# Optimization experiments

Measured on AMD Instinct MI355X. Metric: run time of the kernel, lower is better.

Reference implementation:

```python
import jax, jax.numpy as jnp
import numpy as np

NQ = 100000  # Query nodes
NP = 100000  # Product nodes
E = 600000   # edges per relation
D_IN = 128
D_H = 128
# relation r: (src_type, dst_type); 0=Query, 1=Product
# 0: Click Q->P, 1: reverse_Click P->Q, 2: reverse_QueryResult P->Q, 3: QueryResult Q->P
REL = [(0, 1), (1, 0), (1, 0), (0, 1)]
N_NODES = [NQ, NP]


def setup_inputs() -> dict:
    key = jax.random.key(0)
    ks = jax.random.split(key, 12)
    s = 1.0 / np.sqrt(D_IN)  # keep activations well-scaled across 2 layers
    return {
        "x_query": jax.random.normal(ks[0], (NQ, D_IN), jnp.float32),
        "x_product": jax.random.normal(ks[1], (NP, D_IN), jnp.float32),
        "src_idx": jax.random.randint(ks[2], (4, E), 0, NQ, jnp.int32),
        "dst_idx": jax.random.randint(ks[3], (4, E), 0, NP, jnp.int32),
        "W_self1": jax.random.normal(ks[4], (4, D_IN, D_H), jnp.float32) * s,
        "W_neigh1": jax.random.normal(ks[5], (4, D_IN, D_H), jnp.float32) * s,
        "b1": jnp.zeros((4, D_H), jnp.float32),
        "W_self2": jax.random.normal(ks[6], (4, D_H, D_H), jnp.float32) * s,
        "W_neigh2": jax.random.normal(ks[7], (4, D_H, D_H), jnp.float32) * s,
        "b2": jnp.zeros((4, D_H), jnp.float32),
    }


def _hetero_sage_layer(h, W_self, W_neigh, b, src_idx, dst_idx):
    # h: [h_query, h_product]; per-relation SAGEConv(mean), cross-relation sum
    acc = [None, None]
    for r, (s, t) in enumerate(REL):
        nt = N_NODES[t]
        msg = h[s][src_idx[r]]                                   # [E, d] gather
        neigh_sum = jax.ops.segment_sum(msg, dst_idx[r], num_segments=nt)
        deg = jax.ops.segment_sum(jnp.ones((E,), h[s].dtype), dst_idx[r],
                                  num_segments=nt)
        neigh_mean = neigh_sum / jnp.maximum(deg, 1.0)[:, None]
        out = h[t] @ W_self[r] + neigh_mean @ W_neigh[r] + b[r]
        acc[t] = out if acc[t] is None else acc[t] + out
    return acc


def reference(x_query, x_product, src_idx, dst_idx,
              W_self1, W_neigh1, b1, W_self2, W_neigh2, b2):
    h = [x_query, x_product]
    h = _hetero_sage_layer(h, W_self1, W_neigh1, b1, src_idx, dst_idx)
    h = [jax.nn.relu(v) for v in h]  # ReLU only between layers
    h = _hetero_sage_layer(h, W_self2, W_neigh2, b2, src_idx, dst_idx)
    return (h[0], h[1])  # (H_query, H_product)
```

## Files before the change

kernel.cpp:

```cpp
#include <hip/hip_runtime.h>
#include <hip/hip_bf16.h>

#define N_NODES 100000
#define NEDGE   600000
#define BSHIFT  9
#define NBUCK   196
#define BCAP    3456
#define CGRID   6250
#define WGRID   96

typedef __attribute__((ext_vector_type(8))) short bf16x8;
typedef __attribute__((ext_vector_type(4))) short s16x4;
typedef __attribute__((ext_vector_type(4))) float f32x4;
typedef __attribute__((ext_vector_type(4))) unsigned u32x4;

__device__ __forceinline__ short f2bf(float f) {
  union { float f; unsigned u; } x; x.f = f;
  unsigned r = x.u + 0x7FFFu + ((x.u >> 16) & 1u);
  return (short)(r >> 16);
}

__device__ __forceinline__ unsigned cvtpk(float lo, float hi) {
  unsigned r;
  asm("v_cvt_pk_bf16_f32 %0, %1, %2" : "=v"(r) : "v"(lo), "v"(hi));
  return r;
}

__global__ __launch_bounds__(256) void bin_k(const int* __restrict__ sidx,
                                             const int* __restrict__ didx,
                                             int* __restrict__ bincnt,
                                             unsigned* __restrict__ stage) {
  __shared__ int hist[NBUCK];
  __shared__ int base[NBUCK];
  int r = blockIdx.y, t = threadIdx.x;
  int e0 = blockIdx.x * 2048 + t;
  const int* dd = didx + (size_t)r * NEDGE;
  const int* ss = sidx + (size_t)r * NEDGE;
  for (int i = t; i < NBUCK; i += 256) hist[i] = 0;
  __syncthreads();
  unsigned pv[8]; int bu[8], lr[8];
#pragma unroll
  for (int j = 0; j < 8; ++j) {
    int e = e0 + j * 256;
    if (e < NEDGE) {
      int dv = dd[e];
      bu[j] = dv >> BSHIFT;
      pv[j] = (unsigned)ss[e] | ((unsigned)(dv & 511) << 17);
      lr[j] = atomicAdd(&hist[bu[j]], 1);
    }
  }
  __syncthreads();
  for (int i = t; i < NBUCK; i += 256)
    base[i] = atomicAdd(&bincnt[r * NBUCK + i], hist[i]);
  __syncthreads();
#pragma unroll
  for (int j = 0; j < 8; ++j) {
    int e = e0 + j * 256;
    if (e < NEDGE)
      stage[(size_t)(r * NBUCK + bu[j]) * BCAP + base[bu[j]] + lr[j]] = pv[j];
  }
}

__global__ __launch_bounds__(256) void hist_k(const unsigned* __restrict__ stage,
                                              const int* __restrict__ bincnt,
                                              int* __restrict__ cnt,
                                              int* __restrict__ bucketsum) {
  __shared__ int h[512];
  __shared__ int red[256];
  int bu = blockIdx.x, r = blockIdx.y, t = threadIdx.x;
  int len = bincnt[r * NBUCK + bu];
  const unsigned* sg = stage + (size_t)(r * NBUCK + bu) * BCAP;
  h[t] = 0; h[t + 256] = 0;
  __syncthreads();
  for (int i = t; i < len; i += 256) atomicAdd(&h[sg[i] >> 17], 1);
  __syncthreads();
  int lo = bu << BSHIFT;
  int d0 = lo + t;
  if (d0 < N_NODES)       cnt[r * N_NODES + d0]       = h[t];
  if (d0 + 256 < N_NODES) cnt[r * N_NODES + d0 + 256] = h[t + 256];
  red[t] = h[t] + h[t + 256];
  __syncthreads();
  for (int st = 128; st > 0; st >>= 1) {
    if (t < st) red[t] += red[t + st];
    __syncthreads();
  }
  if (t == 0) bucketsum[r * NBUCK + bu] = red[0];
}

__global__ __launch_bounds__(256) void scan2_k(int* __restrict__ bucketsum) {
  __shared__ int buf[256];
  int t = threadIdx.x;
  for (int r = 0; r < 4; ++r) {
    int v = (t < NBUCK) ? bucketsum[r * NBUCK + t] : 0;
    buf[t] = v;
    __syncthreads();
    for (int st = 1; st < 256; st <<= 1) {
      int x = (t >= st) ? buf[t - st] : 0;
      __syncthreads();
      buf[t] += x;
      __syncthreads();
    }
    if (t < NBUCK) bucketsum[r * NBUCK + t] = buf[t] - v;
    __syncthreads();
  }
}

__global__ __launch_bounds__(256) void scan3_k(const int* __restrict__ cnt,
                                               const int* __restrict__ bucketsum,
                                               int* __restrict__ off) {
  __shared__ int ps[256];
  int bu = blockIdx.x, r = blockIdx.y, t = threadIdx.x;
  int lo = bu << BSHIFT;
  int i0 = lo + 2 * t;
  int c0 = (i0 < N_NODES) ? cnt[r * N_NODES + i0] : 0;
  int c1 = (i0 + 1 < N_NODES) ? cnt[r * N_NODES + i0 + 1] : 0;
  int pair = c0 + c1;
  ps[t] = pair;
  __syncthreads();
  for (int st = 1; st < 256; st <<= 1) {
    int x = (t >= st) ? ps[t - st] : 0;
    __syncthreads();
    ps[t] += x;
    __syncthreads();
  }
  int base = bucketsum[r * NBUCK + bu] + ps[t] - pair;
  int* o = off + r * (N_NODES + 1);
  if (i0 < N_NODES)     o[i0]     = base;
  if (i0 + 1 < N_NODES) o[i0 + 1] = base + c0;
  if (bu == 0 && t == 0) o[N_NODES] = NEDGE;
}

__global__ __launch_bounds__(256) void place_k(const unsigned* __restrict__ stage,
                                               const int* __restrict__ bincnt,
                                               const int* __restrict__ off,
                                               int* __restrict__ csr) {
  __shared__ int ofl[512];
  __shared__ int cur[512];
  int bu = blockIdx.x, r = blockIdx.y, t = threadIdx.x;
  int len = bincnt[r * NBUCK + bu];
  const unsigned* sg = stage + (size_t)(r * NBUCK + bu) * BCAP;
  const int* of = off + r * (N_NODES + 1);
  int* cs = csr + (size_t)r * NEDGE;
  int lo = bu << BSHIFT;
  int d0 = lo + t;
  ofl[t]       = (d0 < N_NODES) ? of[d0] : 0;
  ofl[t + 256] = (d0 + 256 < N_NODES) ? of[d0 + 256] : 0;
  cur[t] = 0; cur[t + 256] = 0;
  __syncthreads();
  for (int i = t; i < len; i += 256) {
    unsigned v = sg[i];
    int dl = v >> 17;
    int pos = ofl[dl] + atomicAdd(&cur[dl], 1);
    cs[pos] = (int)(v & 0x1FFFFu);
  }
}

__global__ __launch_bounds__(256) void fatprep_k(
    const float* __restrict__ xq, const float* __restrict__ xp,
    unsigned* __restrict__ xqb, unsigned* __restrict__ xpb,
    const float* __restrict__ Ws1, const float* __restrict__ Wn1,
    const float* __restrict__ Ws2, const float* __restrict__ Wn2,
    short* __restrict__ WTp,
    const float* __restrict__ b1, const float* __restrict__ b2,
    float* __restrict__ biasc) {
  int b = blockIdx.x, t = threadIdx.x;
  if (b < 2 * CGRID) {
    const float* x = (b < CGRID) ? xq : xp;
    unsigned* o = (b < CGRID) ? xqb : xpb;
    int i = (b < CGRID ? b : b - CGRID) * 256 + t;
    f32x4 v0 = ((const f32x4*)x)[i * 2];
    f32x4 v1 = ((const f32x4*)x)[i * 2 + 1];
    ((u32x4*)o)[i] = (u32x4){cvtpk(v0[0], v0[1]), cvtpk(v0[2], v0[3]),
                             cvtpk(v1[0], v1[1]), cvtpk(v1[2], v1[3])};
  } else if (b < 2 * CGRID + WGRID) {
    int tid = (b - 2 * CGRID) * 256 + t;
    int lane = tid & 63;
    int n0 = (tid >> 6) & 7;
    int idx3 = tid >> 9;
    int k0 = idx3 % 12;
    int lt = idx3 / 12;
    int l = lt >> 1, ty = lt & 1;
    const float* Wself  = l ? Ws2 : Ws1;
    const float* Wneigh = l ? Wn2 : Wn1;
    int rA = ty ? 0 : 1, rB = ty ? 3 : 2;
    int n = n0 * 16 + (lane & 15);
    int kbase = k0 * 32 + (lane >> 4) * 8;
    short out[8];
#pragma unroll
    for (int j = 0; j < 8; ++j) {
      int k = kbase + j;
      int kk = k & 127, blk = k >> 7;
      float v;
      if (blk == 0)      v = Wself[rA * 16384 + kk * 128 + n] + Wself[rB * 16384 + kk * 128 + n];
      else if (blk == 1) v = Wneigh[rA * 16384 + kk * 128 + n];
      else               v = Wneigh[rB * 16384 + kk * 128 + n];
      out[j] = f2bf(v);
    }
    s16x4* dst = (s16x4*)&WTp[tid * 8];
    dst[0] = *(s16x4*)&out[0];
    dst[1] = *(s16x4*)&out[4];
  } else {
#pragma unroll
    for (int q = 0; q < 2; ++q) {
      int tid = t + q * 256;
      int l = tid >> 8, ty = (tid >> 7) & 1, c = tid & 127;
      const float* bb = l ? b2 : b1;
      int rA = ty ? 0 : 1, rB = ty ? 3 : 2;
      biasc[tid] = bb[rA * 128 + c] + bb[rB * 128 + c];
    }
  }
}

#define ACC8(u, a)                                            \
  {                                                           \
    _Pragma("unroll") for (int q = 0; q < 4; ++q) {           \
      union { unsigned w; float f; } lo_, hi_;                \
      lo_.w = (u)[q] << 16; hi_.w = (u)[q] & 0xffff0000u;     \
      (a)[2 * q] += lo_.f; (a)[2 * q + 1] += hi_.f;           \
    }                                                         \
  }

__device__ __forceinline__ int clampi(int q, int p0, int p1) {
  int t = q < p1 ? q : p0;
  return t < NEDGE ? t : 0;
}

__global__ __launch_bounds__(256) void gather2_k(
    const unsigned* __restrict__ src0, const unsigned* __restrict__ src1,
    const int* __restrict__ csr, const int* __restrict__ off,
    unsigned* __restrict__ m00, unsigned* __restrict__ m01,
    unsigned* __restrict__ m10, unsigned* __restrict__ m11) {
  int wv = __builtin_amdgcn_readfirstlane(threadIdx.x >> 6);
  int wid = blockIdx.x * 4 + wv;
  int lane = threadIdx.x & 63;
  int type = wid >= N_NODES;
  int n = type ? wid - N_NODES : wid;
  const unsigned* src = type ? src1 : src0;
  const int* csrA = csr + (type ? 0 : 1) * NEDGE;
  const int* csrB = csr + (type ? 3 : 2) * NEDGE;
  const int* offA = off + (type ? 0 : 1) * (N_NODES + 1);
  const int* offB = off + (type ? 3 : 2) * (N_NODES + 1);
  unsigned* mA = type ? m10 : m00;
  unsigned* mB = type ? m11 : m01;
  int pA0 = offA[n], pA1 = offA[n + 1];
  int pB0 = offB[n], pB1 = offB[n + 1];
  int degA = pA1 - pA0, degB = pB1 - pB0;
  int rowg = lane >> 4;
  int colg = lane & 15;
  float a[8] = {}, b[8] = {};
  {
    int ia0 = csrA[clampi(pA0 + rowg,     pA0, pA1)];
    int ia1 = csrA[clampi(pA0 + 4 + rowg, pA0, pA1)];
    int ib0 = csrB[clampi(pB0 + rowg,     pB0, pB1)];
    int ib1 = csrB[clampi(pB0 + 4 + rowg, pB0, pB1)];
    u32x4 ua0 = *(const u32x4*)(src + (size_t)ia0 * 64 + colg * 4);
    u32x4 ua1 = *(const u32x4*)(src + (size_t)ia1 * 64 + colg * 4);
    u32x4 ub0 = *(const u32x4*)(src + (size_t)ib0 * 64 + colg * 4);
    u32x4 ub1 = *(const u32x4*)(src + (size_t)ib1 * 64 + colg * 4);
    if (pA0 + rowg     < pA1) ACC8(ua0, a);
    if (pA0 + 4 + rowg < pA1) ACC8(ua1, a);
    if (pB0 + rowg     < pB1) ACC8(ub0, b);
    if (pB0 + 4 + rowg < pB1) ACC8(ub1, b);
  }
  for (int p = pA0 + 8; p < pA1; p += 8) {
    int i0 = csrA[clampi(p + rowg,     pA0, pA1)];
    int i1 = csrA[clampi(p + 4 + rowg, pA0, pA1)];
    u32x4 u0 = *(const u32x4*)(src + (size_t)i0 * 64 + colg * 4);
    u32x4 u1 = *(const u32x4*)(src + (size_t)i1 * 64 + colg * 4);
    if (p + rowg     < pA1) ACC8(u0, a);
    if (p + 4 + rowg < pA1) ACC8(u1, a);
  }
  for (int p = pB0 + 8; p < pB1; p += 8) {
    int i0 = csrB[clampi(p + rowg,     pB0, pB1)];
    int i1 = csrB[clampi(p + 4 + rowg, pB0, pB1)];
    u32x4 u0 = *(const u32x4*)(src + (size_t)i0 * 64 + colg * 4);
    u32x4 u1 = *(const u32x4*)(src + (size_t)i1 * 64 + colg * 4);
    if (p + rowg     < pB1) ACC8(u0, b);
    if (p + 4 + rowg < pB1) ACC8(u1, b);
  }
#pragma unroll
  for (int q = 0; q < 8; ++q) {
    a[q] += __shfl_xor(a[q], 16); a[q] += __shfl_xor(a[q], 32);
    b[q] += __shfl_xor(b[q], 16); b[q] += __shfl_xor(b[q], 32);
  }
  if (rowg == 0) {
    float invA = 1.0f / (float)(degA > 1 ? degA : 1);
    float invB = 1.0f / (float)(degB > 1 ? degB : 1);
    u32x4 wa, wb;
#pragma unroll
    for (int q = 0; q < 4; ++q) {
      wa[q] = cvtpk(a[2 * q] * invA, a[2 * q + 1] * invA);
      wb[q] = cvtpk(b[2 * q] * invB, b[2 * q + 1] * invB);
    }
    *(u32x4*)(mA + (size_t)n * 64 + colg * 4) = wa;
    *(u32x4*)(mB + (size_t)n * 64 + colg * 4) = wb;
  }
}

template<int OUT_RELU_BF16>
__global__ __launch_bounds__(256) void gemm2_k(
    const short* __restrict__ self0, const short* __restrict__ self1,
    const short* __restrict__ mA0, const short* __restrict__ mB0,
    const short* __restrict__ mA1, const short* __restrict__ mB1,
    const short* __restrict__ WTpL, const float* __restrict__ biascL,
    void* __restrict__ out0, void* __restrict__ out1) {
  __shared__ short Wlds[2][8192];
  int type = blockIdx.y;
  const short* selfp = type ? self1 : self0;
  const short* meanA = type ? mA1 : mA0;
  const short* meanB = type ? mB1 : mB0;
  const short* WTp = WTpL + type * 49152;
  const float* biasc = biascL + type * 128;
  void* outp = type ? out1 : out0;
  int tid = threadIdx.x;
  int lane = tid & 63, wave = tid >> 6;
  int rowbase = blockIdx.x * 128 + wave * 32;
  int r0 = rowbase + (lane & 15), r1 = r0 + 16;
  int rc0 = r0 < N_NODES ? r0 : N_NODES - 1;
  int rc1 = r1 < N_NODES ? r1 : N_NODES - 1;
  int kg = lane >> 4;
  f32x4 acc[2][8] = {};
  const f32x4* Wsrc = (const f32x4*)WTp;
  f32x4 st[4];
#pragma unroll
  for (int j = 0; j < 4; ++j) st[j] = Wsrc[tid + j * 256];
  {
    f32x4* d = (f32x4*)Wlds[0];
#pragma unroll
    for (int j = 0; j < 4; ++j) d[tid + j * 256] = st[j];
  }
  __syncthreads();
  for (int c = 0; c < 6; ++c) {
    if (c < 5) {
#pragma unroll
      for (int j = 0; j < 4; ++j) st[j] = Wsrc[(c + 1) * 1024 + tid + j * 256];
    }
    const short* mp = (c < 2) ? selfp : ((c < 4) ? meanA : meanB);
    const short* wbase = Wlds[c & 1];
#pragma unroll
    for (int kh = 0; kh < 2; ++kh) {
      int kk = (c * 2 + kh) & 3;
      int kin = kk * 32 + kg * 8;
      bf16x8 a0 = *(const bf16x8*)(mp + (size_t)rc0 * 128 + kin);
      bf16x8 a1 = *(const bf16x8*)(mp + (size_t)rc1 * 128 + kin);
      const short* wb = wbase + kh * 4096 + lane * 8;
#pragma unroll
      for (int n0 = 0; n0 < 8; ++n0) {
        bf16x8 b = *(const bf16x8*)(wb + n0 * 512);
        acc[0][n0] = __builtin_amdgcn_mfma_f32_16x16x32_bf16(a0, b, acc[0][n0], 0, 0, 0);
        acc[1][n0] = __builtin_amdgcn_mfma_f32_16x16x32_bf16(a1, b, acc[1][n0], 0, 0, 0);
      }
    }
    if (c < 5) {
      f32x4* d = (f32x4*)Wlds[(c + 1) & 1];
#pragma unroll
      for (int j = 0; j < 4; ++j) d[tid + j * 256] = st[j];
    }
    __syncthreads();
  }
  int colb = lane & 15, rloc = kg * 4;
#pragma unroll
  for (int mt = 0; mt < 2; ++mt) {
    int rb = rowbase + mt * 16 + rloc;
#pragma unroll
    for (int n0 = 0; n0 < 8; ++n0) {
      int cc = n0 * 16 + colb;
      float bv = biasc[cc];
#pragma unroll
      for (int j = 0; j < 4; ++j) {
        int rr = rb + j;
        if (rr < N_NODES) {
          float v = acc[mt][n0][j] + bv;
          if (OUT_RELU_BF16) {
            ((short*)outp)[(size_t)rr * 128 + cc] = f2bf(v > 0.f ? v : 0.f);
          } else {
            __builtin_nontemporal_store(v, (float*)outp + (size_t)rr * 128 + cc);
          }
        }
      }
    }
  }
}

extern "C" void kernel_launch(void* const* d_in, const int* in_sizes, int n_in,
                              void* d_out, int out_size, void* d_ws, size_t ws_size,
                              hipStream_t stream) {
  (void)in_sizes; (void)n_in; (void)out_size; (void)ws_size;
  const float* xq  = (const float*)d_in[0];
  const float* xp  = (const float*)d_in[1];
  const int*   src = (const int*)d_in[2];
  const int*   dst = (const int*)d_in[3];
  const float* Ws1 = (const float*)d_in[4];
  const float* Wn1 = (const float*)d_in[5];
  const float* b1  = (const float*)d_in[6];
  const float* Ws2 = (const float*)d_in[7];
  const float* Wn2 = (const float*)d_in[8];
  const float* b2  = (const float*)d_in[9];

  char* w = (char*)d_ws;
  int*   cnt    = (int*)w;      w += (size_t)4 * N_NODES * 4;
  int*   bincnt = (int*)w;      w += 4096;
  int*   bsum   = (int*)w;      w += 4 * 256 * 4;
  int*   off    = (int*)w;      w += (size_t)4 * (N_NODES + 1) * 4;
  int*   csr    = (int*)w;      w += (size_t)4 * NEDGE * 4;
  short* meanA  = (short*)w;    w += (size_t)N_NODES * 128 * 2;
  short* meanB  = (short*)w;    w += (size_t)N_NODES * 128 * 2;
  short* h1q    = (short*)w;    w += (size_t)N_NODES * 128 * 2;
  short* h1p    = (short*)w;    w += (size_t)N_NODES * 128 * 2;
  short* xqb    = (short*)w;    w += (size_t)N_NODES * 128 * 2;
  short* xpb    = (short*)w;    w += (size_t)N_NODES * 128 * 2;
  short* WTp    = (short*)w;    w += (size_t)4 * 49152 * 2;
  float* biasc  = (float*)w;    w += 512 * 4;
  unsigned* stage = (unsigned*)meanA;
  unsigned* mL1C = (unsigned*)d_out;
  unsigned* mL1D = mL1C + (size_t)N_NODES * 64;
  unsigned* mL2C = (unsigned*)xqb;
  unsigned* mL2D = (unsigned*)xpb;

  dim3 b256(256);
  const int bgrid = (NEDGE + 2047) / 2048;
  const int ggrid = (N_NODES + 127) / 128;
  const int wgrid = 2 * N_NODES / 4;

  hipMemsetAsync(bincnt, 0, 4096, stream);
  bin_k<<<dim3(bgrid, 4), b256, 0, stream>>>(src, dst, bincnt, stage);
  hist_k<<<dim3(NBUCK, 4), b256, 0, stream>>>(stage, bincnt, cnt, bsum);
  scan2_k<<<dim3(1), b256, 0, stream>>>(bsum);
  scan3_k<<<dim3(NBUCK, 4), b256, 0, stream>>>(cnt, bsum, off);
  place_k<<<dim3(NBUCK, 4), b256, 0, stream>>>(stage, bincnt, off, csr);
  fatprep_k<<<dim3(2 * CGRID + WGRID + 1), b256, 0, stream>>>(
      xq, xp, (unsigned*)xqb, (unsigned*)xpb,
      Ws1, Wn1, Ws2, Wn2, WTp, b1, b2, biasc);

  gather2_k<<<wgrid, b256, 0, stream>>>((const unsigned*)xpb, (const unsigned*)xqb,
      csr, off, (unsigned*)meanA, (unsigned*)meanB, mL1C, mL1D);
  gemm2_k<1><<<dim3(ggrid, 2), b256, 0, stream>>>(
      xqb, xpb, meanA, meanB, (const short*)mL1C, (const short*)mL1D,
      WTp, biasc, h1q, h1p);

  gather2_k<<<wgrid, b256, 0, stream>>>((const unsigned*)h1p, (const unsigned*)h1q,
      csr, off, (unsigned*)meanA, (unsigned*)meanB, mL2C, mL2D);
  gemm2_k<0><<<dim3(ggrid, 2), b256, 0, stream>>>(
      h1q, h1p, meanA, meanB, (const short*)mL2C, (const short*)mL2D,
      WTp + 2 * 49152, biasc + 256,
      (float*)d_out, (float*)d_out + (size_t)N_NODES * 128);
}
```

Baseline: 461.6 us.

## Fuse binning with prep, merge scan and place, halve GEMM row tile

Edge binning is folded into the fat prep kernel as extra leading blocks, and the per-bucket scan and placement kernels are merged so the offsets stay in shared memory. Together these cut two kernel launches and the global reread of offsets. The GEMM now gives each wave 16 rows instead of 32, doubling the grid for more parallelism at the cost of less weight reuse per block. Fusing bin and prep puts atomic binning work into the same launch as the bandwidth-bound conversion.

Result: faster. 452.1 us (-2.1%).

```diff
diff --git a/kernel.cpp b/kernel.cpp
--- a/kernel.cpp
+++ b/kernel.cpp
@@ -8,6 +8,7 @@
 #define BCAP    3456
 #define CGRID   6250
 #define WGRID   96
+#define BINGRID 1172
 
 typedef __attribute__((ext_vector_type(8))) short bf16x8;
 typedef __attribute__((ext_vector_type(4))) short s16x4;
@@ -26,136 +27,9 @@
   return r;
 }
 
-__global__ __launch_bounds__(256) void bin_k(const int* __restrict__ sidx,
-                                             const int* __restrict__ didx,
-                                             int* __restrict__ bincnt,
-                                             unsigned* __restrict__ stage) {
-  __shared__ int hist[NBUCK];
-  __shared__ int base[NBUCK];
-  int r = blockIdx.y, t = threadIdx.x;
-  int e0 = blockIdx.x * 2048 + t;
-  const int* dd = didx + (size_t)r * NEDGE;
-  const int* ss = sidx + (size_t)r * NEDGE;
-  for (int i = t; i < NBUCK; i += 256) hist[i] = 0;
-  __syncthreads();
-  unsigned pv[8]; int bu[8], lr[8];
-#pragma unroll
-  for (int j = 0; j < 8; ++j) {
-    int e = e0 + j * 256;
-    if (e < NEDGE) {
-      int dv = dd[e];
-      bu[j] = dv >> BSHIFT;
-      pv[j] = (unsigned)ss[e] | ((unsigned)(dv & 511) << 17);
-      lr[j] = atomicAdd(&hist[bu[j]], 1);
-    }
-  }
-  __syncthreads();
-  for (int i = t; i < NBUCK; i += 256)
-    base[i] = atomicAdd(&bincnt[r * NBUCK + i], hist[i]);
-  __syncthreads();
-#pragma unroll
-  for (int j = 0; j < 8; ++j) {
-    int e = e0 + j * 256;
-    if (e < NEDGE)
-      stage[(size_t)(r * NBUCK + bu[j]) * BCAP + base[bu[j]] + lr[j]] = pv[j];
-  }
-}
-
-__global__ __launch_bounds__(256) void hist_k(const unsigned* __restrict__ stage,
-                                              const int* __restrict__ bincnt,
-                                              int* __restrict__ cnt,
-                                              int* __restrict__ bucketsum) {
-  __shared__ int h[512];
-  __shared__ int red[256];
-  int bu = blockIdx.x, r = blockIdx.y, t = threadIdx.x;
-  int len = bincnt[r * NBUCK + bu];
-  const unsigned* sg = stage + (size_t)(r * NBUCK + bu) * BCAP;
-  h[t] = 0; h[t + 256] = 0;
-  __syncthreads();
-  for (int i = t; i < len; i += 256) atomicAdd(&h[sg[i] >> 17], 1);
-  __syncthreads();
-  int lo = bu << BSHIFT;
-  int d0 = lo + t;
-  if (d0 < N_NODES)       cnt[r * N_NODES + d0]       = h[t];
-  if (d0 + 256 < N_NODES) cnt[r * N_NODES + d0 + 256] = h[t + 256];
-  red[t] = h[t] + h[t + 256];
-  __syncthreads();
-  for (int st = 128; st > 0; st >>= 1) {
-    if (t < st) red[t] += red[t + st];
-    __syncthreads();
-  }
-  if (t == 0) bucketsum[r * NBUCK + bu] = red[0];
-}
-
-__global__ __launch_bounds__(256) void scan2_k(int* __restrict__ bucketsum) {
-  __shared__ int buf[256];
-  int t = threadIdx.x;
-  for (int r = 0; r < 4; ++r) {
-    int v = (t < NBUCK) ? bucketsum[r * NBUCK + t] : 0;
-    buf[t] = v;
-    __syncthreads();
-    for (int st = 1; st < 256; st <<= 1) {
-      int x = (t >= st) ? buf[t - st] : 0;
-      __syncthreads();
-      buf[t] += x;
-      __syncthreads();
-    }
-    if (t < NBUCK) bucketsum[r * NBUCK + t] = buf[t] - v;
-    __syncthreads();
-  }
-}
-
-__global__ __launch_bounds__(256) void scan3_k(const int* __restrict__ cnt,
-                                               const int* __restrict__ bucketsum,
-                                               int* __restrict__ off) {
-  __shared__ int ps[256];
-  int bu = blockIdx.x, r = blockIdx.y, t = threadIdx.x;
-  int lo = bu << BSHIFT;
-  int i0 = lo + 2 * t;
-  int c0 = (i0 < N_NODES) ? cnt[r * N_NODES + i0] : 0;
-  int c1 = (i0 + 1 < N_NODES) ? cnt[r * N_NODES + i0 + 1] : 0;
-  int pair = c0 + c1;
-  ps[t] = pair;
-  __syncthreads();
-  for (int st = 1; st < 256; st <<= 1) {
-    int x = (t >= st) ? ps[t - st] : 0;
-    __syncthreads();
-    ps[t] += x;
-    __syncthreads();
-  }
-  int base = bucketsum[r * NBUCK + bu] + ps[t] - pair;
-  int* o = off + r * (N_NODES + 1);
-  if (i0 < N_NODES)     o[i0]     = base;
-  if (i0 + 1 < N_NODES) o[i0 + 1] = base + c0;
-  if (bu == 0 && t == 0) o[N_NODES] = NEDGE;
-}
-
-__global__ __launch_bounds__(256) void place_k(const unsigned* __restrict__ stage,
-                                               const int* __restrict__ bincnt,
-                                               const int* __restrict__ off,
-                                               int* __restrict__ csr) {
-  __shared__ int ofl[512];
-  __shared__ int cur[512];
-  int bu = blockIdx.x, r = blockIdx.y, t = threadIdx.x;
-  int len = bincnt[r * NBUCK + bu];
-  const unsigned* sg = stage + (size_t)(r * NBUCK + bu) * BCAP;
-  const int* of = off + r * (N_NODES + 1);
-  int* cs = csr + (size_t)r * NEDGE;
-  int lo = bu << BSHIFT;
-  int d0 = lo + t;
-  ofl[t]       = (d0 < N_NODES) ? of[d0] : 0;
-  ofl[t + 256] = (d0 + 256 < N_NODES) ? of[d0 + 256] : 0;
-  cur[t] = 0; cur[t + 256] = 0;
-  __syncthreads();
-  for (int i = t; i < len; i += 256) {
-    unsigned v = sg[i];
-    int dl = v >> 17;
-    int pos = ofl[dl] + atomicAdd(&cur[dl], 1);
-    cs[pos] = (int)(v & 0x1FFFFu);
-  }
-}
-
-__global__ __launch_bounds__(256) void fatprep_k(
+__global__ __launch_bounds__(256) void bin_fatprep_k(
+    const int* __restrict__ sidx, const int* __restrict__ didx,
+    int* __restrict__ bincnt, unsigned* __restrict__ stage,
     const float* __restrict__ xq, const float* __restrict__ xp,
     unsigned* __restrict__ xqb, unsigned* __restrict__ xpb,
     const float* __restrict__ Ws1, const float* __restrict__ Wn1,
@@ -163,7 +37,40 @@
     short* __restrict__ WTp,
     const float* __restrict__ b1, const float* __restrict__ b2,
     float* __restrict__ biasc) {
-  int b = blockIdx.x, t = threadIdx.x;
+  __shared__ int hist[NBUCK];
+  __shared__ int base[NBUCK];
+  int bb = blockIdx.x, t = threadIdx.x;
+  if (bb < BINGRID) {
+    int r = bb & 3, c = bb >> 2;
+    int e0 = c * 2048 + t;
+    const int* dd = didx + (size_t)r * NEDGE;
+    const int* ss = sidx + (size_t)r * NEDGE;
+    for (int i = t; i < NBUCK; i += 256) hist[i] = 0;
+    __syncthreads();
+    unsigned pv[8]; int bu[8], lr[8];
+#pragma unroll
+    for (int j = 0; j < 8; ++j) {
+      int e = e0 + j * 256;
+      if (e < NEDGE) {
+        int dv = dd[e];
+        bu[j] = dv >> BSHIFT;
+        pv[j] = (unsigned)ss[e] | ((unsigned)(dv & 511) << 17);
+        lr[j] = atomicAdd(&hist[bu[j]], 1);
+      }
+    }
+    __syncthreads();
+    for (int i = t; i < NBUCK; i += 256)
+      base[i] = atomicAdd(&bincnt[r * NBUCK + i], hist[i]);
+    __syncthreads();
+#pragma unroll
+    for (int j = 0; j < 8; ++j) {
+      int e = e0 + j * 256;
+      if (e < NEDGE)
+        stage[(size_t)(r * NBUCK + bu[j]) * BCAP + base[bu[j]] + lr[j]] = pv[j];
+    }
+    return;
+  }
+  int b = bb - BINGRID;
   if (b < 2 * CGRID) {
     const float* x = (b < CGRID) ? xq : xp;
     unsigned* o = (b < CGRID) ? xqb : xpb;
@@ -204,10 +111,95 @@
     for (int q = 0; q < 2; ++q) {
       int tid = t + q * 256;
       int l = tid >> 8, ty = (tid >> 7) & 1, c = tid & 127;
-      const float* bb = l ? b2 : b1;
+      const float* bbp = l ? b2 : b1;
       int rA = ty ? 0 : 1, rB = ty ? 3 : 2;
-      biasc[tid] = bb[rA * 128 + c] + bb[rB * 128 + c];
-    }
+      biasc[tid] = bbp[rA * 128 + c] + bbp[rB * 128 + c];
+    }
+  }
+}
+
+__global__ __launch_bounds__(256) void hist_k(const unsigned* __restrict__ stage,
+                                              const int* __restrict__ bincnt,
+                                              int* __restrict__ cnt,
+                                              int* __restrict__ bucketsum) {
+  __shared__ int h[512];
+  __shared__ int red[256];
+  int bu = blockIdx.x, r = blockIdx.y, t = threadIdx.x;
+  int len = bincnt[r * NBUCK + bu];
+  const unsigned* sg = stage + (size_t)(r * NBUCK + bu) * BCAP;
+  h[t] = 0; h[t + 256] = 0;
+  __syncthreads();
+  for (int i = t; i < len; i += 256) atomicAdd(&h[sg[i] >> 17], 1);
+  __syncthreads();
+  int lo = bu << BSHIFT;
+  int d0 = lo + t;
+  if (d0 < N_NODES)       cnt[r * N_NODES + d0]       = h[t];
+  if (d0 + 256 < N_NODES) cnt[r * N_NODES + d0 + 256] = h[t + 256];
+  red[t] = h[t] + h[t + 256];
+  __syncthreads();
+  for (int st = 128; st > 0; st >>= 1) {
+    if (t < st) red[t] += red[t + st];
+    __syncthreads();
+  }
+  if (t == 0) bucketsum[r * NBUCK + bu] = red[0];
+}
+
+__global__ __launch_bounds__(256) void scan2_k(int* __restrict__ bucketsum) {
+  __shared__ int buf[256];
+  int t = threadIdx.x;
+  for (int r = 0; r < 4; ++r) {
+    int v = (t < NBUCK) ? bucketsum[r * NBUCK + t] : 0;
+    buf[t] = v;
+    __syncthreads();
+    for (int st = 1; st < 256; st <<= 1) {
+      int x = (t >= st) ? buf[t - st] : 0;
+      __syncthreads();
+      buf[t] += x;
+      __syncthreads();
+    }
+    if (t < NBUCK) bucketsum[r * NBUCK + t] = buf[t] - v;
+    __syncthreads();
+  }
+}
+
+__global__ __launch_bounds__(256) void scan3place_k(
+    const int* __restrict__ cnt, const int* __restrict__ bucketsum,
+    const unsigned* __restrict__ stage, const int* __restrict__ bincnt,
+    int* __restrict__ off, int* __restrict__ csr) {
+  __shared__ int ps[256];
+  __shared__ int ofl[512];
+  __shared__ int cur[512];
+  int bu = blockIdx.x, r = blockIdx.y, t = threadIdx.x;
+  int lo = bu << BSHIFT;
+  int i0 = lo + 2 * t;
+  int c0 = (i0 < N_NODES) ? cnt[r * N_NODES + i0] : 0;
+  int c1 = (i0 + 1 < N_NODES) ? cnt[r * N_NODES + i0 + 1] : 0;
+  int pair = c0 + c1;
+  ps[t] = pair;
+  __syncthreads();
+  for (int st = 1; st < 256; st <<= 1) {
+    int x = (t >= st) ? ps[t - st] : 0;
+    __syncthreads();
+    ps[t] += x;
+    __syncthreads();
+  }
+  int base = bucketsum[r * NBUCK + bu] + ps[t] - pair;
+  int* o = off + r * (N_NODES + 1);
+  if (i0 < N_NODES)     o[i0]     = base;
+  if (i0 + 1 < N_NODES) o[i0 + 1] = base + c0;
+  if (bu == 0 && t == 0) o[N_NODES] = NEDGE;
+  ofl[2 * t] = base;
+  ofl[2 * t + 1] = base + c0;
+  cur[t] = 0; cur[t + 256] = 0;
+  __syncthreads();
+  int len = bincnt[r * NBUCK + bu];
+  const unsigned* sg = stage + (size_t)(r * NBUCK + bu) * BCAP;
+  int* cs = csr + (size_t)r * NEDGE;
+  for (int i = t; i < len; i += 256) {
+    unsigned v = sg[i];
+    int dl = v >> 17;
+    int pos = ofl[dl] + atomicAdd(&cur[dl], 1);
+    cs[pos] = (int)(v & 0x1FFFFu);
   }
 }
 
@@ -314,12 +306,11 @@
   void* outp = type ? out1 : out0;
   int tid = threadIdx.x;
   int lane = tid & 63, wave = tid >> 6;
-  int rowbase = blockIdx.x * 128 + wave * 32;
-  int r0 = rowbase + (lane & 15), r1 = r0 + 16;
+  int rowbase = blockIdx.x * 64 + wave * 16;
+  int r0 = rowbase + (lane & 15);
   int rc0 = r0 < N_NODES ? r0 : N_NODES - 1;
-  int rc1 = r1 < N_NODES ? r1 : N_NODES - 1;
   int kg = lane >> 4;
-  f32x4 acc[2][8] = {};
+  f32x4 acc[8] = {};
   const f32x4* Wsrc = (const f32x4*)WTp;
   f32x4 st[4];
 #pragma unroll
@@ -342,13 +333,11 @@
       int kk = (c * 2 + kh) & 3;
       int kin = kk * 32 + kg * 8;
       bf16x8 a0 = *(const bf16x8*)(mp + (size_t)rc0 * 128 + kin);
-      bf16x8 a1 = *(const bf16x8*)(mp + (size_t)rc1 * 128 + kin);
       const short* wb = wbase + kh * 4096 + lane * 8;
 #pragma unroll
       for (int n0 = 0; n0 < 8; ++n0) {
         bf16x8 b = *(const bf16x8*)(wb + n0 * 512);
-        acc[0][n0] = __builtin_amdgcn_mfma_f32_16x16x32_bf16(a0, b, acc[0][n0], 0, 0, 0);
-        acc[1][n0] = __builtin_amdgcn_mfma_f32_16x16x32_bf16(a1, b, acc[1][n0], 0, 0, 0);
+        acc[n0] = __builtin_amdgcn_mfma_f32_16x16x32_bf16(a0, b, acc[n0], 0, 0, 0);
       }
     }
     if (c < 5) {
@@ -359,23 +348,20 @@
     __syncthreads();
   }
   int colb = lane & 15, rloc = kg * 4;
-#pragma unroll
-  for (int mt = 0; mt < 2; ++mt) {
-    int rb = rowbase + mt * 16 + rloc;
-#pragma unroll
-    for (int n0 = 0; n0 < 8; ++n0) {
-      int cc = n0 * 16 + colb;
-      float bv = biasc[cc];
-#pragma unroll
-      for (int j = 0; j < 4; ++j) {
-        int rr = rb + j;
-        if (rr < N_NODES) {
-          float v = acc[mt][n0][j] + bv;
-          if (OUT_RELU_BF16) {
-            ((short*)outp)[(size_t)rr * 128 + cc] = f2bf(v > 0.f ? v : 0.f);
-          } else {
-            __builtin_nontemporal_store(v, (float*)outp + (size_t)rr * 128 + cc);
-          }
+  int rb = rowbase + rloc;
+#pragma unroll
+  for (int n0 = 0; n0 < 8; ++n0) {
+    int cc = n0 * 16 + colb;
+    float bv = biasc[cc];
+#pragma unroll
+    for (int j = 0; j < 4; ++j) {
+      int rr = rb + j;
+      if (rr < N_NODES) {
+        float v = acc[n0][j] + bv;
+        if (OUT_RELU_BF16) {
+          ((short*)outp)[(size_t)rr * 128 + cc] = f2bf(v > 0.f ? v : 0.f);
+        } else {
+          __builtin_nontemporal_store(v, (float*)outp + (size_t)rr * 128 + cc);
         }
       }
     }
@@ -418,19 +404,17 @@
   unsigned* mL2D = (unsigned*)xpb;
 
   dim3 b256(256);
-  const int bgrid = (NEDGE + 2047) / 2048;
-  const int ggrid = (N_NODES + 127) / 128;
+  const int ggrid = (N_NODES + 63) / 64;
   const int wgrid = 2 * N_NODES / 4;
 
   hipMemsetAsync(bincnt, 0, 4096, stream);
-  bin_k<<<dim3(bgrid, 4), b256, 0, stream>>>(src, dst, bincnt, stage);
+  bin_fatprep_k<<<dim3(BINGRID + 2 * CGRID + WGRID + 1), b256, 0, stream>>>(
+      src, dst, bincnt, stage, xq, xp, (unsigned*)xqb, (unsigned*)xpb,
+      Ws1, Wn1, Ws2, Wn2, WTp, b1, b2, biasc);
   hist_k<<<dim3(NBUCK, 4), b256, 0, stream>>>(stage, bincnt, cnt, bsum);
   scan2_k<<<dim3(1), b256, 0, stream>>>(bsum);
-  scan3_k<<<dim3(NBUCK, 4), b256, 0, stream>>>(cnt, bsum, off);
-  place_k<<<dim3(NBUCK, 4), b256, 0, stream>>>(stage, bincnt, off, csr);
-  fatprep_k<<<dim3(2 * CGRID + WGRID + 1), b256, 0, stream>>>(
-      xq, xp, (unsigned*)xqb, (unsigned*)xpb,
-      Ws1, Wn1, Ws2, Wn2, WTp, b1, b2, biasc);
+  scan3place_k<<<dim3(NBUCK, 4), b256, 0, stream>>>(cnt, bsum, stage, bincnt,
+                                                    off, csr);
 
   gather2_k<<<wgrid, b256, 0, stream>>>((const unsigned*)xpb, (const unsigned*)xqb,
       csr, off, (unsigned*)meanA, (unsigned*)meanB, mL1C, mL1D);
```
